# Performance work log

Measured on AMD Instinct MI355X. Metric: run time of the kernel, lower is better.

Reference implementation:

```python
import jax, jax.numpy as jnp
import numpy as np

B, L = 1, 2048
D_MODEL, N_LAYER, D_INNER = 768, 2, 1536
D_STATE, DT_RANK, D_CONV, OUT_DIM = 16, 48, 4, 128


def setup_inputs() -> dict:
    key = jax.random.key(0)
    ks = jax.random.split(key, 10)
    s = 0.02
    p = {}
    p["x"] = jax.random.normal(ks[0], (B, L, D_MODEL), jnp.float32)
    # stacked per-layer parameters, leading dim = N_LAYER
    p["in_proj_w"] = jax.random.normal(ks[1], (N_LAYER, 2 * D_INNER, D_MODEL), jnp.float32) * s
    p["conv_w"] = jax.random.normal(ks[2], (N_LAYER, D_INNER, D_CONV), jnp.float32) * s
    p["conv_b"] = jnp.zeros((N_LAYER, D_INNER), jnp.float32)
    p["x_proj_w"] = jax.random.normal(ks[3], (N_LAYER, DT_RANK + 2 * D_STATE, D_INNER), jnp.float32) * s
    p["dt_proj_w"] = jax.random.normal(ks[4], (N_LAYER, D_INNER, DT_RANK), jnp.float32) * s
    p["dt_proj_b"] = jax.random.normal(ks[5], (N_LAYER, D_INNER), jnp.float32) * s
    A = jnp.tile(jnp.arange(1, D_STATE + 1, dtype=jnp.float32)[None, :], (D_INNER, 1))
    p["A_log"] = jnp.tile(jnp.log(A)[None], (N_LAYER, 1, 1))
    p["D"] = jnp.ones((N_LAYER, D_INNER), jnp.float32)
    p["out_proj_w"] = jax.random.normal(ks[6], (N_LAYER, D_MODEL, D_INNER), jnp.float32) * s
    p["norm_w"] = jnp.ones((N_LAYER, D_MODEL), jnp.float32)
    p["norm_f_w"] = jnp.ones((D_MODEL,), jnp.float32)
    p["head_w"] = jax.random.normal(ks[7], (OUT_DIM, D_MODEL), jnp.float32) * s
    return p


def rmsnorm(x, w, eps=1e-5):
    return x * jax.lax.rsqrt(jnp.mean(x * x, -1, keepdims=True) + eps) * w


def selective_scan(u, delta, A, Bm, Cm, Dv):
    # u, delta: (b,l,d); A: (d,n); Bm, Cm: (b,l,n); Dv: (d,)
    dA = jnp.exp(jnp.einsum('bld,dn->bldn', delta, A))       # discretized A
    dBu = jnp.einsum('bld,bln->bldn', delta * u, Bm)          # discretized B*u

    def step(s, inp):
        dA_t, dBu_t, C_t = inp                               # (b,d,n),(b,d,n),(b,n)
        s = dA_t * s + dBu_t
        y = jnp.einsum('bdn,bn->bd', s, C_t)
        return s, y

    s0 = jnp.zeros((u.shape[0], u.shape[2], A.shape[1]), u.dtype)
    _, ys = jax.lax.scan(step, s0, (dA.transpose(1, 0, 2, 3), dBu.transpose(1, 0, 2, 3), Cm.transpose(1, 0, 2)))
    y = ys.transpose(1, 0, 2)                                # (b,l,d)
    return y + u * Dv


def mamba_block(x, w):
    xr = jnp.einsum('bld,ed->ble', x, w['in_proj_w'])        # (b,l,2*d_inner)
    xin, res = jnp.split(xr, 2, axis=-1)
    # causal depthwise conv1d
    xc = jax.lax.conv_general_dilated(
        xin.transpose(0, 2, 1), w['conv_w'][:, None, :],
        window_strides=(1,), padding=[(D_CONV - 1, 0)],
        dimension_numbers=('NCH', 'OIH', 'NCH'),
        feature_group_count=D_INNER)
    xc = (xc + w['conv_b'][None, :, None]).transpose(0, 2, 1)
    xc = jax.nn.silu(xc)
    # SSM
    A = -jnp.exp(w['A_log'])                                 # (d_inner, d_state)
    proj = jnp.einsum('bld,ed->ble', xc, w['x_proj_w'])
    delta, Bm, Cm = jnp.split(proj, [DT_RANK, DT_RANK + D_STATE], axis=-1)
    delta = jax.nn.softplus(jnp.einsum('blr,dr->bld', delta, w['dt_proj_w']) + w['dt_proj_b'])
    y = selective_scan(xc, delta, A, Bm, Cm, w['D'])
    y = y * jax.nn.silu(res)
    return jnp.einsum('bld,ed->ble', y, w['out_proj_w'])


def reference(x, in_proj_w, conv_w, conv_b, x_proj_w, dt_proj_w, dt_proj_b,
              A_log, D, out_proj_w, norm_w, norm_f_w, head_w):
    stacked = dict(in_proj_w=in_proj_w, conv_w=conv_w, conv_b=conv_b,
                   x_proj_w=x_proj_w, dt_proj_w=dt_proj_w, dt_proj_b=dt_proj_b,
                   A_log=A_log, D=D, out_proj_w=out_proj_w)
    for i in range(N_LAYER):
        w = {k: v[i] for k, v in stacked.items()}
        x = x + mamba_block(rmsnorm(x, norm_w[i]), w)        # pre-norm residual block
    x = rmsnorm(x, norm_f_w)
    return jnp.einsum('bld,od->blo', x, head_w)              # lm_head (no bias)
```

## Files before the change

kernel.cpp:

```cpp
#include <hip/hip_runtime.h>
#include <hip/hip_bf16.h>
#include <stdint.h>

#define LSEQ 2048
#define DM 768
#define DI 1536
#define NCH 128
#define CHK 16

typedef __bf16 bf16;
typedef short short8 __attribute__((ext_vector_type(8)));
typedef float floatx4 __attribute__((ext_vector_type(4)));
typedef bf16 bf16x8 __attribute__((ext_vector_type(8)));

__device__ inline float silu_f(float x){ return x / (1.f + __expf(-x)); }

__device__ __forceinline__ void g2l16(const bf16* g, bf16* l){
  __builtin_amdgcn_global_load_lds(
      (const __attribute__((address_space(1))) void*)g,
      (__attribute__((address_space(3))) void*)l, 16, 0, 0);
}

__device__ inline int bf16_flag(const void* dvv){
  return (*(const unsigned*)dvv == 0x3F803F80u) ? 1 : 0;
}

__device__ inline float ldin(const void* p, long i, int f){
  return f ? (float)((const bf16*)p)[i] : ((const float*)p)[i];
}

__device__ __forceinline__ void ld8(const void* src, long i, int f, float* o){
  if(f){
    bf16x8 v = *(const bf16x8*)((const bf16*)src + i);
    #pragma unroll
    for(int k = 0; k < 8; k++) o[k] = (float)v[k];
  } else {
    float4 a = ((const float4*)src)[i >> 2];
    float4 b = ((const float4*)src)[(i >> 2) + 1];
    o[0]=a.x; o[1]=a.y; o[2]=a.z; o[3]=a.w; o[4]=b.x; o[5]=b.y; o[6]=b.z; o[7]=b.w;
  }
}
__device__ __forceinline__ void st8_bf(bf16* dst, long i, const float* o){
  bf16x8 v;
  #pragma unroll
  for(int k = 0; k < 8; k++) v[k] = (bf16)o[k];
  *(bf16x8*)(dst + i) = v;
}
__device__ __forceinline__ void st8_f32(float* dst, long i, const float* o){
  ((float4*)dst)[i >> 2]       = make_float4(o[0], o[1], o[2], o[3]);
  ((float4*)dst)[(i >> 2) + 1] = make_float4(o[4], o[5], o[6], o[7]);
}

#define NB_INW  2304
#define NB_OUTW 1152
#define NB_HW   48
#define NB_X    768
#define NB_ALOG 24
#define NB_XPW  192
#define NB_DTW  96
#define NB_SM   12
#define NB_TOT  (NB_INW+NB_OUTW+NB_HW+NB_X+NB_ALOG+NB_XPW+NB_DTW+NB_SM)

__global__ __launch_bounds__(256) void k_canon(const void* x_, const void* inw_,
    const void* cw_, const void* cb_, const void* xpw_, const void* dtw_,
    const void* dtb_, const void* dvv_, const void* alog_, const void* outw_,
    const void* nw_, const void* nfw_, const void* hw_,
    float* x0, bf16* inw, float* cw, float* cb, bf16* xpw, bf16* dtw, float* dtb,
    float* alog, float* dv, bf16* outw, float* nw, float* nfw, bf16* hw){
  int f = bf16_flag(dvv_);
  int b = blockIdx.x;
  int t = threadIdx.x;
  float o[8];
  if(b < NB_INW + NB_OUTW + NB_HW){
    const void* src; bf16* dst; long off;
    if(b < NB_INW){ src = inw_; dst = inw; off = (long)b*2048; }
    else if(b < NB_INW + NB_OUTW){ src = outw_; dst = outw; off = (long)(b - NB_INW)*2048; }
    else { src = hw_; dst = hw; off = (long)(b - NB_INW - NB_OUTW)*2048; }
    long i = off + t*8;
    if(f){ *(bf16x8*)(dst + i) = *(const bf16x8*)((const bf16*)src + i); }
    else { ld8(src, i, 0, o); st8_bf(dst, i, o); }
    return;
  }
  b -= NB_INW + NB_OUTW + NB_HW;
  if(b < NB_X + NB_ALOG){
    const void* src; float* dst; long off;
    if(b < NB_X){ src = x_; dst = x0; off = (long)b*2048; }
    else { src = alog_; dst = alog; off = (long)(b - NB_X)*2048; }
    long i = off + t*8;
    ld8(src, i, f, o);
    st8_f32(dst, i, o);
    return;
  }
  b -= NB_X + NB_ALOG;
  if(b < NB_XPW){
    long j = (long)b*2048 + t*8;
    int layer = (int)(j / (128*DI));
    int rem = (int)(j % (128*DI));
    int r = rem / DI, c = rem % DI;
    if(r < 80){
      ld8(xpw_, ((long)layer*80 + r)*DI + c, f, o);
    } else {
      for(int k = 0; k < 8; k++) o[k] = 0.f;
    }
    st8_bf(xpw, j, o);
    return;
  }
  b -= NB_XPW;
  if(b < NB_DTW){
    long j = (long)b*2048 + t*8;
    int layer = (int)(j / (DI*64));
    int rem = (int)(j % (DI*64));
    int r = rem / 64, c = rem % 64;
    if(c < 48){
      ld8(dtw_, ((long)layer*DI + r)*48 + c, f, o);
    } else {
      for(int k = 0; k < 8; k++) o[k] = 0.f;
    }
    st8_bf(dtw, j, o);
    return;
  }
  b -= NB_DTW;
  for(int idx = b*256 + t; idx < 23808; idx += NB_SM*256){
    int j = idx;
    if(j < 12288){ cw[j] = ldin(cw_, j, f); continue; } j -= 12288;
    if(j < 3072){ cb[j] = ldin(cb_, j, f); continue; } j -= 3072;
    if(j < 3072){ dtb[j] = ldin(dtb_, j, f); continue; } j -= 3072;
    if(j < 3072){ dv[j] = ldin(dvv_, j, f); continue; } j -= 3072;
    if(j < 1536){ nw[j] = ldin(nw_, j, f); continue; } j -= 1536;
    nfw[j] = ldin(nfw_, j, f);
  }
}

__global__ __launch_bounds__(256) void k_rmsnorm(const float* __restrict__ x,
    const float* __restrict__ w, bf16* __restrict__ out){
  int row = blockIdx.x;
  const float* xr = x + row*DM;
  int t = threadIdx.x;
  float v0 = xr[t], v1 = xr[t+256], v2 = xr[t+512];
  float ss = v0*v0 + v1*v1 + v2*v2;
  #pragma unroll
  for(int o = 32; o; o >>= 1) ss += __shfl_down(ss, o, 64);
  __shared__ float red[4];
  int lane = t & 63, wid = t >> 6;
  if(lane == 0) red[wid] = ss;
  __syncthreads();
  ss = red[0] + red[1] + red[2] + red[3];
  float rs = rsqrtf(ss / DM + 1e-5f);
  out[row*DM + t]       = (bf16)(v0 * rs * w[t]);
  out[row*DM + t + 256] = (bf16)(v1 * rs * w[t+256]);
  out[row*DM + t + 512] = (bf16)(v2 * rs * w[t+512]);
}

template<int SPLITK, int MODE>
__global__ __launch_bounds__(256) void k_gemm(
    const bf16* __restrict__ A, const bf16* __restrict__ B, float* __restrict__ C,
    int K, int ldc, const float* __restrict__ aux){
  __shared__ bf16 sA[128*32];
  __shared__ bf16 sB[128*32];
  int bm0 = blockIdx.y*128, bn0 = blockIdx.x*128;
  int tid = threadIdx.x;
  int lane = tid & 63, wid = tid >> 6;
  int wm = (wid >> 1)*64, wn = (wid & 1)*64;
  int quad = lane >> 4, lr = lane & 15;
  const int klen = K / SPLITK;
  const int kbeg = (SPLITK > 1) ? blockIdx.z * klen : 0;
  const bf16* Ag = A + (size_t)(bm0 + (tid>>2))*K + kbeg + (tid&3)*8;
  const bf16* Bg = B + (size_t)(bn0 + (tid>>2))*K + kbeg + (tid&3)*8;
  bf16* lA0 = sA + tid*8;
  bf16* lA1 = sA + 2048 + tid*8;
  bf16* lB0 = sB + tid*8;
  bf16* lB1 = sB + 2048 + tid*8;
  floatx4 acc[4][4] = {};
  for(int k0 = 0; k0 < klen; k0 += 32){
    __syncthreads();
    g2l16(Ag, lA0); g2l16(Ag + 64*K, lA1);
    g2l16(Bg, lB0); g2l16(Bg + 64*K, lB1);
    __syncthreads();
    short8 af[4], bf_[4];
    #pragma unroll
    for(int i = 0; i < 4; i++){
      af[i]  = *(const short8*)(sA + (wm + i*16 + lr)*32 + quad*8);
      bf_[i] = *(const short8*)(sB + (wn + i*16 + lr)*32 + quad*8);
    }
    #pragma unroll
    for(int i = 0; i < 4; i++)
      #pragma unroll
      for(int j = 0; j < 4; j++)
        acc[i][j] = __builtin_amdgcn_mfma_f32_16x16x32_bf16(af[i], bf_[j], acc[i][j], 0, 0, 0);
    Ag += 32; Bg += 32;
  }
  float* Co = C + ((MODE == 5) ? (size_t)blockIdx.z * LSEQ * ldc : 0);
  #pragma unroll
  for(int i = 0; i < 4; i++){
    #pragma unroll
    for(int j = 0; j < 4; j++){
      #pragma unroll
      for(int r = 0; r < 4; r++){
        int grow = bm0 + wm + i*16 + quad*4 + r;
        int gcol = bn0 + wn + j*16 + lr;
        float v = acc[i][j][r];
        if(MODE == 1){
          v += aux[gcol];
          v = fmaxf(v, 0.f) + log1pf(__expf(-fabsf(v)));
        }
        Co[(size_t)grow*ldc + gcol] = v;
      }
    }
  }
  (void)aux;
}

__global__ __launch_bounds__(256) void k_epi_xproj(const float* __restrict__ part,
    float* __restrict__ proj, bf16* __restrict__ dtin){
  int idx = blockIdx.x*256 + threadIdx.x;
  float s = 0.f;
  #pragma unroll
  for(int z = 0; z < 8; z++) s += part[(size_t)z*LSEQ*128 + idx];
  int row = idx >> 7, col = idx & 127;
  if(col < 80) proj[row*80 + col] = s;
  if(col < 64) dtin[row*64 + col] = (col < 48) ? (bf16)s : (bf16)0.f;
}

__global__ __launch_bounds__(256) void k_epi_out_norm(const float* __restrict__ part,
    const float* __restrict__ resid, const float* __restrict__ w,
    float* __restrict__ xws, bf16* __restrict__ xn){
  int row = blockIdx.x;
  int t = threadIdx.x;
  float v[3]; float ss = 0.f;
  #pragma unroll
  for(int k = 0; k < 3; k++){
    long i = (long)row*DM + t + k*256;
    float s = part[i] + part[(long)LSEQ*DM + i] + resid[i];
    xws[i] = s; v[k] = s; ss += s*s;
  }
  #pragma unroll
  for(int o = 32; o; o >>= 1) ss += __shfl_down(ss, o, 64);
  __shared__ float red[4];
  if((t & 63) == 0) red[t >> 6] = ss;
  __syncthreads();
  ss = red[0] + red[1] + red[2] + red[3];
  float rs = rsqrtf(ss / DM + 1e-5f);
  #pragma unroll
  for(int k = 0; k < 3; k++){
    int col = t + k*256;
    xn[(long)row*DM + col] = (bf16)(v[k] * rs * w[col]);
  }
}

__global__ __launch_bounds__(256) void k_epi_head(const float* __restrict__ part,
    const void* dvv, void* out){
  int idx = blockIdx.x*256 + threadIdx.x;
  const int N = LSEQ*128;
  float s = part[idx] + part[N+idx] + part[2*N+idx] + part[3*N+idx];
  if(bf16_flag(dvv)) ((bf16*)out)[idx] = (bf16)s;
  else               ((float*)out)[idx] = s;
}

__global__ __launch_bounds__(256) void k_conv(const float* __restrict__ xr,
    const float* __restrict__ cw, const float* __restrict__ cb,
    bf16* __restrict__ xcb){
  int d = blockIdx.x*256 + threadIdx.x;
  int l0 = blockIdx.y*16;
  float w0 = cw[d*4+0], w1 = cw[d*4+1], w2 = cw[d*4+2], w3 = cw[d*4+3];
  float bias = cb[d];
  float xm3 = (l0 >= 3) ? xr[(l0-3)*(2*DI) + d] : 0.f;
  float xm2 = (l0 >= 2) ? xr[(l0-2)*(2*DI) + d] : 0.f;
  float xm1 = (l0 >= 1) ? xr[(l0-1)*(2*DI) + d] : 0.f;
  #pragma unroll
  for(int tl = 0; tl < 16; tl++){
    int l = l0 + tl;
    float xc = xr[l*(2*DI) + d];
    float acc = bias + xm3*w0 + xm2*w1 + xm1*w2 + xc*w3;
    xcb[l*DI + d] = (bf16)silu_f(acc);
    xm3 = xm2; xm2 = xm1; xm1 = xc;
  }
}

__global__ __launch_bounds__(256) void k_scan1(
    const float* __restrict__ delta, const bf16* __restrict__ u,
    const float* __restrict__ proj, const float* __restrict__ alog,
    float* __restrict__ Aprod, float* __restrict__ Bsum){
  int d = blockIdx.y*256 + threadIdx.x;
  int c = blockIdx.x;
  __shared__ float Bl[CHK*16];
  {
    int t = threadIdx.x >> 4, n = threadIdx.x & 15;
    Bl[threadIdx.x] = proj[(c*CHK + t)*80 + 48 + n];
  }
  __syncthreads();
  const float L2E = 1.44269504f;
  float An2[16], ap[16], s[16];
  #pragma unroll
  for(int n = 0; n < 16; n++){ An2[n] = -__expf(alog[d*16+n]) * L2E; ap[n] = 1.f; s[n] = 0.f; }
  int t0 = c*CHK;
  float dt = delta[t0*DI + d];
  float uu = (float)u[t0*DI + d];
  #pragma unroll
  for(int tl = 0; tl < CHK; tl++){
    float dtn = 0.f, un = 0.f;
    if(tl + 1 < CHK){
      dtn = delta[(t0+tl+1)*DI + d];
      un = (float)u[(t0+tl+1)*DI + d];
    }
    float du = dt * uu;
    #pragma unroll
    for(int n = 0; n < 16; n++){
      float e = exp2f(dt * An2[n]);
      s[n] = e*s[n] + du*Bl[tl*16+n];
      ap[n] *= e;
    }
    dt = dtn; uu = un;
  }
  int base = (c*DI + d)*16;
  #pragma unroll
  for(int n = 0; n < 16; n++){ Aprod[base+n] = ap[n]; Bsum[base+n] = s[n]; }
}

__global__ __launch_bounds__(256) void k_scan2(float* __restrict__ Aprod,
    const float* __restrict__ Bsum){
  int idx = blockIdx.x*256 + threadIdx.x;
  float s = 0.f;
  for(int c = 0; c < NCH; c++){
    int o = c*DI*16 + idx;
    float a = Aprod[o], b = Bsum[o];
    Aprod[o] = s;
    s = a*s + b;
  }
}

__global__ __launch_bounds__(256) void k_scan3(
    const float* __restrict__ delta, const bf16* __restrict__ u,
    const float* __restrict__ proj, const float* __restrict__ alog,
    const float* __restrict__ dvp, const float* __restrict__ Sinit,
    const float* __restrict__ xr, bf16* __restrict__ ybar){
  int d = blockIdx.y*256 + threadIdx.x;
  int c = blockIdx.x;
  __shared__ float Bl[CHK*16], Cl[CHK*16];
  {
    int t = threadIdx.x >> 4, n = threadIdx.x & 15;
    Bl[threadIdx.x] = proj[(c*CHK + t)*80 + 48 + n];
    Cl[threadIdx.x] = proj[(c*CHK + t)*80 + 64 + n];
  }
  __syncthreads();
  const float L2E = 1.44269504f;
  float An2[16], s[16];
  #pragma unroll
  for(int n = 0; n < 16; n++) An2[n] = -__expf(alog[d*16+n]) * L2E;
  int base = (c*DI + d)*16;
  #pragma unroll
  for(int n = 0; n < 16; n++) s[n] = Sinit[base+n];
  float Dd = dvp[d];
  int t0 = c*CHK;
  float dt = delta[t0*DI + d];
  float uu = (float)u[t0*DI + d];
  float res = xr[t0*(2*DI) + DI + d];
  #pragma unroll
  for(int tl = 0; tl < CHK; tl++){
    float dtn = 0.f, un = 0.f, rn = 0.f;
    if(tl + 1 < CHK){
      dtn = delta[(t0+tl+1)*DI + d];
      un = (float)u[(t0+tl+1)*DI + d];
      rn = xr[(t0+tl+1)*(2*DI) + DI + d];
    }
    float du = dt * uu;
    float y = 0.f;
    #pragma unroll
    for(int n = 0; n < 16; n++){
      float e = exp2f(dt * An2[n]);
      s[n] = e*s[n] + du*Bl[tl*16+n];
      y += s[n]*Cl[tl*16+n];
    }
    y += uu * Dd;
    ybar[(t0+tl)*DI + d] = (bf16)(y * silu_f(res));
    dt = dtn; uu = un; res = rn;
  }
}

extern "C" void kernel_launch(void* const* d_in, const int* in_sizes, int n_in,
                              void* d_out, int out_size, void* d_ws, size_t ws_size,
                              hipStream_t stream){
  const void* x_   = d_in[0];
  const void* inw_ = d_in[1];
  const void* cw_  = d_in[2];
  const void* cb_  = d_in[3];
  const void* xpw_ = d_in[4];
  const void* dtw_ = d_in[5];
  const void* dtb_ = d_in[6];
  const void* alog_= d_in[7];
  const void* dvv_ = d_in[8];
  const void* outw_= d_in[9];
  const void* nw_  = d_in[10];
  const void* nfw_ = d_in[11];
  const void* hw_  = d_in[12];

  char* p = (char*)d_ws;
  auto alloc = [&](size_t n){ char* r = p; p += (n + 255) & ~(size_t)255; return r; };
  float* x0  = (float*)alloc((size_t)LSEQ*DM*4);
  bf16* inw  = (bf16*)alloc((size_t)2*2*DI*DM*2);
  float* cw  = (float*)alloc((size_t)2*DI*4*4);
  float* cb  = (float*)alloc((size_t)2*DI*4);
  bf16* xpw  = (bf16*)alloc((size_t)2*128*DI*2);
  bf16* dtw  = (bf16*)alloc((size_t)2*DI*64*2);
  float* dtb = (float*)alloc((size_t)2*DI*4);
  float* alog= (float*)alloc((size_t)2*DI*16*4);
  float* dv  = (float*)alloc((size_t)2*DI*4);
  bf16* outw = (bf16*)alloc((size_t)2*DM*DI*2);
  float* nw  = (float*)alloc((size_t)2*DM*4);
  float* nfw = (float*)alloc((size_t)DM*4);
  bf16* hw   = (bf16*)alloc((size_t)128*DM*2);
  bf16* xn   = (bf16*)alloc((size_t)LSEQ*DM*2);
  float* xr  = (float*)alloc((size_t)LSEQ*2*DI*4);
  bf16* xcb  = (bf16*)alloc((size_t)LSEQ*DI*2);
  float* proj= (float*)alloc((size_t)LSEQ*80*4);
  bf16* dtin = (bf16*)alloc((size_t)LSEQ*64*2);
  float* delta=(float*)alloc((size_t)LSEQ*DI*4);
  float* Aprod=(float*)alloc((size_t)NCH*DI*16*4);
  float* Bsum =(float*)alloc((size_t)NCH*DI*16*4);
  bf16* ybar = (bf16*)alloc((size_t)LSEQ*DI*2);
  float* xws = (float*)alloc((size_t)LSEQ*DM*4);
  float* part = delta;

  k_canon<<<NB_TOT, 256, 0, stream>>>(x_, inw_, cw_, cb_, xpw_, dtw_, dtb_, dvv_,
      alog_, outw_, nw_, nfw_, hw_,
      x0, inw, cw, cb, xpw, dtw, dtb, alog, dv, outw, nw, nfw, hw);

  k_rmsnorm<<<LSEQ, 256, 0, stream>>>(x0, nw, xn);
  const float* xcur = x0;
  for(int i = 0; i < 2; i++){
    k_gemm<1,0><<<dim3(2*DI/128, LSEQ/128), 256, 0, stream>>>(
        xn, inw + (size_t)i*2*DI*DM, xr, DM, 2*DI, nullptr);
    k_conv<<<dim3(DI/256, LSEQ/16), 256, 0, stream>>>(xr, cw + i*DI*4, cb + i*DI, xcb);
    k_gemm<8,5><<<dim3(1, LSEQ/128, 8), 256, 0, stream>>>(
        xcb, xpw + (size_t)i*128*DI, part, DI, 128, nullptr);
    k_epi_xproj<<<LSEQ*128/256, 256, 0, stream>>>(part, proj, dtin);
    k_gemm<1,1><<<dim3(DI/128, LSEQ/128), 256, 0, stream>>>(
        dtin, dtw + (size_t)i*DI*64, delta, 64, DI, dtb + i*DI);
    k_scan1<<<dim3(NCH, DI/256), 256, 0, stream>>>(delta, xcb, proj, alog + i*DI*16, Aprod, Bsum);
    k_scan2<<<DI*16/256, 256, 0, stream>>>(Aprod, Bsum);
    k_scan3<<<dim3(NCH, DI/256), 256, 0, stream>>>(delta, xcb, proj, alog + i*DI*16,
        dv + i*DI, Aprod, xr, ybar);
    k_gemm<2,5><<<dim3(DM/128, LSEQ/128, 2), 256, 0, stream>>>(
        ybar, outw + (size_t)i*DM*DI, part, DI, DM, nullptr);
    k_epi_out_norm<<<LSEQ, 256, 0, stream>>>(part, xcur,
        (i == 0) ? (nw + DM) : nfw, xws, xn);
    xcur = xws;
  }
  k_gemm<4,5><<<dim3(1, LSEQ/128, 4), 256, 0, stream>>>(
      xn, hw, part, DM, 128, nullptr);
  k_epi_head<<<LSEQ*128/256, 256, 0, stream>>>(part, dvv_, d_out);

  (void)in_sizes; (void)n_in; (void)out_size; (void)ws_size;
}
```

Before: 411.0 us.

## Store in_proj and delta outputs as bf16 and shrink GEMM tile to 64x128

The in_proj GEMM output (xr) and the dt_proj output (delta) are now written as bf16 instead of fp32, and the conv and scan kernels read bf16. This halves the global memory traffic for these large intermediates. The GEMM tile is also cut from 128x128 to 64x128 with each wave covering 64x32, which doubles the block count for better CU occupancy but lowers data reuse per block. The split-K partial buffer gets its own allocation because delta is now too small to alias it. Rounding xr and delta to bf16 adds precision loss in the scan.

Measured after the change: 380.8 us. 1.08x faster.

```diff
diff --git a/kernel.cpp b/kernel.cpp
--- a/kernel.cpp
+++ b/kernel.cpp
@@ -153,57 +153,60 @@
 
 template<int SPLITK, int MODE>
 __global__ __launch_bounds__(256) void k_gemm(
-    const bf16* __restrict__ A, const bf16* __restrict__ B, float* __restrict__ C,
+    const bf16* __restrict__ A, const bf16* __restrict__ B, void* Cv,
     int K, int ldc, const float* __restrict__ aux){
-  __shared__ bf16 sA[128*32];
+  __shared__ bf16 sA[64*32];
   __shared__ bf16 sB[128*32];
-  int bm0 = blockIdx.y*128, bn0 = blockIdx.x*128;
+  int bm0 = blockIdx.y*64, bn0 = blockIdx.x*128;
   int tid = threadIdx.x;
   int lane = tid & 63, wid = tid >> 6;
-  int wm = (wid >> 1)*64, wn = (wid & 1)*64;
+  int wn = wid*32;
   int quad = lane >> 4, lr = lane & 15;
   const int klen = K / SPLITK;
   const int kbeg = (SPLITK > 1) ? blockIdx.z * klen : 0;
   const bf16* Ag = A + (size_t)(bm0 + (tid>>2))*K + kbeg + (tid&3)*8;
   const bf16* Bg = B + (size_t)(bn0 + (tid>>2))*K + kbeg + (tid&3)*8;
-  bf16* lA0 = sA + tid*8;
-  bf16* lA1 = sA + 2048 + tid*8;
-  bf16* lB0 = sB + tid*8;
-  bf16* lB1 = sB + 2048 + tid*8;
-  floatx4 acc[4][4] = {};
+  floatx4 acc[4][2] = {};
   for(int k0 = 0; k0 < klen; k0 += 32){
     __syncthreads();
-    g2l16(Ag, lA0); g2l16(Ag + 64*K, lA1);
-    g2l16(Bg, lB0); g2l16(Bg + 64*K, lB1);
+    g2l16(Ag, sA + tid*8);
+    g2l16(Bg, sB + tid*8);
+    g2l16(Bg + 64*K, sB + 2048 + tid*8);
     __syncthreads();
-    short8 af[4], bf_[4];
-    #pragma unroll
-    for(int i = 0; i < 4; i++){
-      af[i]  = *(const short8*)(sA + (wm + i*16 + lr)*32 + quad*8);
-      bf_[i] = *(const short8*)(sB + (wn + i*16 + lr)*32 + quad*8);
-    }
+    short8 af[4], bf_[2];
+    #pragma unroll
+    for(int i = 0; i < 4; i++)
+      af[i]  = *(const short8*)(sA + (i*16 + lr)*32 + quad*8);
+    #pragma unroll
+    for(int j = 0; j < 2; j++)
+      bf_[j] = *(const short8*)(sB + (wn + j*16 + lr)*32 + quad*8);
     #pragma unroll
     for(int i = 0; i < 4; i++)
       #pragma unroll
-      for(int j = 0; j < 4; j++)
+      for(int j = 0; j < 2; j++)
         acc[i][j] = __builtin_amdgcn_mfma_f32_16x16x32_bf16(af[i], bf_[j], acc[i][j], 0, 0, 0);
     Ag += 32; Bg += 32;
   }
-  float* Co = C + ((MODE == 5) ? (size_t)blockIdx.z * LSEQ * ldc : 0);
+  float* Cf = (float*)Cv + ((MODE == 5) ? (size_t)blockIdx.z * LSEQ * ldc : 0);
+  bf16* Cb = (bf16*)Cv;
   #pragma unroll
   for(int i = 0; i < 4; i++){
     #pragma unroll
-    for(int j = 0; j < 4; j++){
+    for(int j = 0; j < 2; j++){
       #pragma unroll
       for(int r = 0; r < 4; r++){
-        int grow = bm0 + wm + i*16 + quad*4 + r;
+        int grow = bm0 + i*16 + quad*4 + r;
         int gcol = bn0 + wn + j*16 + lr;
         float v = acc[i][j][r];
-        if(MODE == 1){
+        if(MODE == 0){
+          Cb[(size_t)grow*ldc + gcol] = (bf16)v;
+        } else if(MODE == 1){
           v += aux[gcol];
           v = fmaxf(v, 0.f) + log1pf(__expf(-fabsf(v)));
+          Cb[(size_t)grow*ldc + gcol] = (bf16)v;
+        } else {
+          Cf[(size_t)grow*ldc + gcol] = v;
         }
-        Co[(size_t)grow*ldc + gcol] = v;
       }
     }
   }
@@ -256,20 +259,20 @@
   else               ((float*)out)[idx] = s;
 }
 
-__global__ __launch_bounds__(256) void k_conv(const float* __restrict__ xr,
+__global__ __launch_bounds__(256) void k_conv(const bf16* __restrict__ xr,
     const float* __restrict__ cw, const float* __restrict__ cb,
     bf16* __restrict__ xcb){
   int d = blockIdx.x*256 + threadIdx.x;
   int l0 = blockIdx.y*16;
   float w0 = cw[d*4+0], w1 = cw[d*4+1], w2 = cw[d*4+2], w3 = cw[d*4+3];
   float bias = cb[d];
-  float xm3 = (l0 >= 3) ? xr[(l0-3)*(2*DI) + d] : 0.f;
-  float xm2 = (l0 >= 2) ? xr[(l0-2)*(2*DI) + d] : 0.f;
-  float xm1 = (l0 >= 1) ? xr[(l0-1)*(2*DI) + d] : 0.f;
+  float xm3 = (l0 >= 3) ? (float)xr[(l0-3)*(2*DI) + d] : 0.f;
+  float xm2 = (l0 >= 2) ? (float)xr[(l0-2)*(2*DI) + d] : 0.f;
+  float xm1 = (l0 >= 1) ? (float)xr[(l0-1)*(2*DI) + d] : 0.f;
   #pragma unroll
   for(int tl = 0; tl < 16; tl++){
     int l = l0 + tl;
-    float xc = xr[l*(2*DI) + d];
+    float xc = (float)xr[l*(2*DI) + d];
     float acc = bias + xm3*w0 + xm2*w1 + xm1*w2 + xc*w3;
     xcb[l*DI + d] = (bf16)silu_f(acc);
     xm3 = xm2; xm2 = xm1; xm1 = xc;
@@ -277,7 +280,7 @@
 }
 
 __global__ __launch_bounds__(256) void k_scan1(
-    const float* __restrict__ delta, const bf16* __restrict__ u,
+    const bf16* __restrict__ delta, const bf16* __restrict__ u,
     const float* __restrict__ proj, const float* __restrict__ alog,
     float* __restrict__ Aprod, float* __restrict__ Bsum){
   int d = blockIdx.y*256 + threadIdx.x;
@@ -293,13 +296,13 @@
   #pragma unroll
   for(int n = 0; n < 16; n++){ An2[n] = -__expf(alog[d*16+n]) * L2E; ap[n] = 1.f; s[n] = 0.f; }
   int t0 = c*CHK;
-  float dt = delta[t0*DI + d];
+  float dt = (float)delta[t0*DI + d];
   float uu = (float)u[t0*DI + d];
   #pragma unroll
   for(int tl = 0; tl < CHK; tl++){
     float dtn = 0.f, un = 0.f;
     if(tl + 1 < CHK){
-      dtn = delta[(t0+tl+1)*DI + d];
+      dtn = (float)delta[(t0+tl+1)*DI + d];
       un = (float)u[(t0+tl+1)*DI + d];
     }
     float du = dt * uu;
@@ -329,10 +332,10 @@
 }
 
 __global__ __launch_bounds__(256) void k_scan3(
-    const float* __restrict__ delta, const bf16* __restrict__ u,
+    const bf16* __restrict__ delta, const bf16* __restrict__ u,
     const float* __restrict__ proj, const float* __restrict__ alog,
     const float* __restrict__ dvp, const float* __restrict__ Sinit,
-    const float* __restrict__ xr, bf16* __restrict__ ybar){
+    const bf16* __restrict__ xr, bf16* __restrict__ ybar){
   int d = blockIdx.y*256 + threadIdx.x;
   int c = blockIdx.x;
   __shared__ float Bl[CHK*16], Cl[CHK*16];
@@ -351,16 +354,16 @@
   for(int n = 0; n < 16; n++) s[n] = Sinit[base+n];
   float Dd = dvp[d];
   int t0 = c*CHK;
-  float dt = delta[t0*DI + d];
+  float dt = (float)delta[t0*DI + d];
   float uu = (float)u[t0*DI + d];
-  float res = xr[t0*(2*DI) + DI + d];
+  float res = (float)xr[t0*(2*DI) + DI + d];
   #pragma unroll
   for(int tl = 0; tl < CHK; tl++){
     float dtn = 0.f, un = 0.f, rn = 0.f;
     if(tl + 1 < CHK){
-      dtn = delta[(t0+tl+1)*DI + d];
+      dtn = (float)delta[(t0+tl+1)*DI + d];
       un = (float)u[(t0+tl+1)*DI + d];
-      rn = xr[(t0+tl+1)*(2*DI) + DI + d];
+      rn = (float)xr[(t0+tl+1)*(2*DI) + DI + d];
     }
     float du = dt * uu;
     float y = 0.f;
@@ -409,16 +412,16 @@
   float* nfw = (float*)alloc((size_t)DM*4);
   bf16* hw   = (bf16*)alloc((size_t)128*DM*2);
   bf16* xn   = (bf16*)alloc((size_t)LSEQ*DM*2);
-  float* xr  = (float*)alloc((size_t)LSEQ*2*DI*4);
+  bf16* xr   = (bf16*)alloc((size_t)LSEQ*2*DI*2);
   bf16* xcb  = (bf16*)alloc((size_t)LSEQ*DI*2);
   float* proj= (float*)alloc((size_t)LSEQ*80*4);
   bf16* dtin = (bf16*)alloc((size_t)LSEQ*64*2);
-  float* delta=(float*)alloc((size_t)LSEQ*DI*4);
+  bf16* delta= (bf16*)alloc((size_t)LSEQ*DI*2);
   float* Aprod=(float*)alloc((size_t)NCH*DI*16*4);
   float* Bsum =(float*)alloc((size_t)NCH*DI*16*4);
   bf16* ybar = (bf16*)alloc((size_t)LSEQ*DI*2);
   float* xws = (float*)alloc((size_t)LSEQ*DM*4);
-  float* part = delta;
+  float* part = (float*)alloc((size_t)2*LSEQ*DM*4);
 
   k_canon<<<NB_TOT, 256, 0, stream>>>(x_, inw_, cw_, cb_, xpw_, dtw_, dtb_, dvv_,
       alog_, outw_, nw_, nfw_, hw_,
@@ -427,25 +430,25 @@
   k_rmsnorm<<<LSEQ, 256, 0, stream>>>(x0, nw, xn);
   const float* xcur = x0;
   for(int i = 0; i < 2; i++){
-    k_gemm<1,0><<<dim3(2*DI/128, LSEQ/128), 256, 0, stream>>>(
+    k_gemm<1,0><<<dim3(2*DI/128, LSEQ/64), 256, 0, stream>>>(
         xn, inw + (size_t)i*2*DI*DM, xr, DM, 2*DI, nullptr);
     k_conv<<<dim3(DI/256, LSEQ/16), 256, 0, stream>>>(xr, cw + i*DI*4, cb + i*DI, xcb);
-    k_gemm<8,5><<<dim3(1, LSEQ/128, 8), 256, 0, stream>>>(
+    k_gemm<8,5><<<dim3(1, LSEQ/64, 8), 256, 0, stream>>>(
         xcb, xpw + (size_t)i*128*DI, part, DI, 128, nullptr);
     k_epi_xproj<<<LSEQ*128/256, 256, 0, stream>>>(part, proj, dtin);
-    k_gemm<1,1><<<dim3(DI/128, LSEQ/128), 256, 0, stream>>>(
+    k_gemm<1,1><<<dim3(DI/128, LSEQ/64), 256, 0, stream>>>(
         dtin, dtw + (size_t)i*DI*64, delta, 64, DI, dtb + i*DI);
     k_scan1<<<dim3(NCH, DI/256), 256, 0, stream>>>(delta, xcb, proj, alog + i*DI*16, Aprod, Bsum);
     k_scan2<<<DI*16/256, 256, 0, stream>>>(Aprod, Bsum);
     k_scan3<<<dim3(NCH, DI/256), 256, 0, stream>>>(delta, xcb, proj, alog + i*DI*16,
         dv + i*DI, Aprod, xr, ybar);
-    k_gemm<2,5><<<dim3(DM/128, LSEQ/128, 2), 256, 0, stream>>>(
+    k_gemm<2,5><<<dim3(DM/128, LSEQ/64, 2), 256, 0, stream>>>(
         ybar, outw + (size_t)i*DM*DI, part, DI, DM, nullptr);
     k_epi_out_norm<<<LSEQ, 256, 0, stream>>>(part, xcur,
         (i == 0) ? (nw + DM) : nfw, xws, xn);
     xcur = xws;
   }
-  k_gemm<4,5><<<dim3(1, LSEQ/128, 4), 256, 0, stream>>>(
+  k_gemm<4,5><<<dim3(1, LSEQ/64, 4), 256, 0, stream>>>(
       xn, hw, part, DM, 128, nullptr);
   k_epi_head<<<LSEQ*128/256, 256, 0, stream>>>(part, dvv_, d_out);
 
```
